# Optimization experiments

Hardware: AMD Instinct MI355X
Metric: run time of the kernel (lower is better)

The kernel has to match this reference:

```python
import jax, jax.numpy as jnp
import numpy as np

B, S, V, F, H = 256, 512, 50000, 64, 256


def setup_inputs() -> dict:
    key = jax.random.key(0)
    ks = jax.random.split(key, 12)
    s_in = 1.0 / np.sqrt(F)
    s_hid = 1.0 / np.sqrt(H)
    return {
        "batch": jax.random.randint(ks[0], (B, S), 0, V),
        "features": jax.random.normal(ks[1], (V, F), jnp.float32),
        "W_ih0": jax.random.normal(ks[2], (H, F), jnp.float32) * s_in,
        "W_hh0": jax.random.normal(ks[3], (H, H), jnp.float32) * s_hid,
        "b_ih0": jax.random.normal(ks[4], (H,), jnp.float32) * s_hid,
        "b_hh0": jax.random.normal(ks[5], (H,), jnp.float32) * s_hid,
        "W_ih1": jax.random.normal(ks[6], (H, H), jnp.float32) * s_hid,
        "W_hh1": jax.random.normal(ks[7], (H, H), jnp.float32) * s_hid,
        "b_ih1": jax.random.normal(ks[8], (H,), jnp.float32) * s_hid,
        "b_hh1": jax.random.normal(ks[9], (H,), jnp.float32) * s_hid,
        "W_out": jax.random.normal(ks[10], (V, H), jnp.float32) * s_hid,
        "b_out": jax.random.normal(ks[11], (V,), jnp.float32) * s_hid,
    }


def _rnn_layer(x, W_ih, W_hh, b_ih, b_hh):
    # x: [B, S, Din] -> [B, S, H]; torch tanh RNN: h_t = tanh(x_t W_ih^T + b_ih + h_{t-1} W_hh^T + b_hh)
    xW = jnp.einsum('bsd,hd->bsh', x, W_ih) + (b_ih + b_hh)  # precompute input projection
    h0 = jnp.zeros((x.shape[0], W_hh.shape[0]), x.dtype)

    def step(h, xt):
        h = jnp.tanh(xt + h @ W_hh.T)
        return h, h

    _, ys = jax.lax.scan(step, h0, jnp.swapaxes(xW, 0, 1))  # scan over time
    return jnp.swapaxes(ys, 0, 1)


def reference(batch, features, W_ih0, W_hh0, b_ih0, b_hh0,
              W_ih1, W_hh1, b_ih1, b_hh1, W_out, b_out):
    # vectorized replacement of the nested per-token gather loop
    full_representation = features[batch]            # [B, S, F]
    h = _rnn_layer(full_representation, W_ih0, W_hh0, b_ih0, b_hh0)
    h = _rnn_layer(h, W_ih1, W_hh1, b_ih1, b_hh1)    # [B, S, H]
    return h[:, -1, :] @ W_out.T + b_out             # [B, V]
```

## Files before the change

### kernel.cpp

```cpp
#include <hip/hip_runtime.h>

#define B_ 256
#define S_ 512
#define V_ 50000
#define F_ 64
#define H_ 256

typedef _Float16 f16;
typedef _Float16 f16x2 __attribute__((ext_vector_type(2)));
typedef _Float16 f16x4 __attribute__((ext_vector_type(4)));
typedef _Float16 f16x8 __attribute__((ext_vector_type(8)));
typedef float f32x4 __attribute__((ext_vector_type(4)));

#define MFMA(a, b, c) __builtin_amdgcn_mfma_f32_16x16x32_f16((a), (b), (c), 0, 0, 0)

__device__ __forceinline__ f16x8 cvt8(const float4 a, const float4 b) {
    f16x8 v;
    v[0] = (f16)a.x; v[1] = (f16)a.y; v[2] = (f16)a.z; v[3] = (f16)a.w;
    v[4] = (f16)b.x; v[5] = (f16)b.y; v[6] = (f16)b.z; v[7] = (f16)b.w;
    return v;
}

__device__ __forceinline__ float fast_tanh(float x) {
    float e = __expf(2.f * x);
    float r = __builtin_amdgcn_rcpf(e + 1.f);
    return __builtin_fmaf(-2.f, r, 1.f);
}

__device__ __forceinline__ f32x4 cvt4f(const f16x4 v) {
    f32x4 r; r[0] = (float)v[0]; r[1] = (float)v[1]; r[2] = (float)v[2]; r[3] = (float)v[3];
    return r;
}
__device__ __forceinline__ f16x4 pack4(const f32x4 a, const f32x4 b) {
    f16x4 r; r[0] = (f16)(a[0] + b[0]); r[1] = (f16)(a[1] + b[1]);
    r[2] = (f16)(a[2] + b[2]); r[3] = (f16)(a[3] + b[3]);
    return r;
}
__device__ __forceinline__ f16x4 tanh4(const f32x4 a, const f32x4 b) {
    f16x4 r;
#pragma unroll
    for (int i = 0; i < 4; ++i) r[i] = (f16)fast_tanh(a[i] + b[i]);
    return r;
}

__global__ void k_init_flags(int* flags) {
    if (threadIdx.x < 128) flags[threadIdx.x] = 0;
}

__global__ __launch_bounds__(512) void k_vocab_proj(
    const float* __restrict__ feat, const float* __restrict__ Wih,
    const float* __restrict__ bi, const float* __restrict__ bh,
    f16* __restrict__ T)
{
    __shared__ char Wl[256 * 128];
    __shared__ char Xl[16 * 128];
    const int tid = threadIdx.x;
    {
        const int n = tid >> 1, k0 = (tid & 1) << 5;
#pragma unroll
        for (int k = k0; k < k0 + 32; k += 8) {
            float4 a = *(const float4*)(Wih + n * F_ + k);
            float4 b = *(const float4*)(Wih + n * F_ + k + 4);
            *(f16x8*)(Wl + n * 128 + (((k >> 3) ^ (n & 7)) << 4)) = cvt8(a, b);
        }
    }
    const int v0 = blockIdx.x * 16;
    {
        const int m = tid >> 5, k = (tid & 31) << 1;
        float2 a = *(const float2*)(feat + (v0 + m) * F_ + k);
        f16x2 v; v[0] = (f16)a.x; v[1] = (f16)a.y;
        *(f16x2*)(Xl + m * 128 + ((((k >> 3) ^ (m & 7)) << 4) | ((k & 7) << 1))) = v;
    }
    __syncthreads();
    const int lane = tid & 63, w = tid >> 6;
    const int q = lane & 15, g = lane >> 4;
#pragma unroll
    for (int nt = 0; nt < 2; ++nt) {
        const int n0 = w * 32 + nt * 16;
        const int nrow = n0 + q;
        float4 b1 = *(const float4*)(bi + n0 + g * 4);
        float4 b2 = *(const float4*)(bh + n0 + g * 4);
        f32x4 acc = {b1.x + b2.x, b1.y + b2.y, b1.z + b2.z, b1.w + b2.w};
#pragma unroll
        for (int kb = 0; kb < 2; ++kb) {
            f16x8 a = *(const f16x8*)(Wl + nrow * 128 + (((kb * 4 + g) ^ (nrow & 7)) << 4));
            f16x8 b = *(const f16x8*)(Xl + q * 128 + (((kb * 4 + g) ^ (q & 7)) << 4));
            acc = MFMA(a, b, acc);
        }
        f16x4 o; o[0] = (f16)acc[0]; o[1] = (f16)acc[1]; o[2] = (f16)acc[2]; o[3] = (f16)acc[3];
        *(f16x4*)(T + (size_t)(v0 + q) * H_ + n0 + g * 4) = o;
    }
}

__global__ __launch_bounds__(512) __attribute__((amdgpu_waves_per_eu(2, 2)))
void k_rnn_split(
    const f16* __restrict__ T, const int* __restrict__ idx,
    const float* __restrict__ Whh0, const float* __restrict__ Wih1,
    const float* __restrict__ bih1, const float* __restrict__ bhh1,
    const float* __restrict__ Whh1,
    f16* __restrict__ pbuf, int* flags, f16* __restrict__ h1out)
{
    __shared__ char hb[2][8192];
    const int wg = blockIdx.x;
    const int tid = threadIdx.x, lane = tid & 63, w = tid >> 6;
    const int q = lane & 15, g = lane >> 4;
    const int ncol = w * 32;
    const int swz = (q & 7) << 4;

    int rbase[2], wbase[2];
#pragma unroll
    for (int p2 = 0; p2 < 2; ++p2)
        rbase[p2] = q * 512 + ((p2 * 64 + g * 16) ^ swz);
#pragma unroll
    for (int tt = 0; tt < 2; ++tt)
        wbase[tt] = q * 512 + (((ncol + tt * 16 + g * 4) * 2) ^ swz);

    const int pr = (wg < 16) ? wg : wg - 16;
    const int brow = pr * 16 + q;
    const size_t prow = (size_t)brow * 512;

#define FRD(kb_, RD_) (*(const f16x8*)(hb[RD_] + rbase[(kb_) & 1] + (((kb_) >> 1) * 128)))
#define HWR(tt_, WR_) (*(f16x4*)(hb[WR_] + wbase[tt_]))
#define STEP_BAR() do { \
        asm volatile("s_waitcnt lgkmcnt(0)" ::: "memory"); \
        __builtin_amdgcn_s_barrier(); \
    } while (0)

    if (wg < 16) {
        f16x8 wA[2][8], wP[2][8];
#pragma unroll
        for (int tt = 0; tt < 2; ++tt) {
            const int n = ncol + tt * 16 + q;
#pragma unroll
            for (int kb = 0; kb < 8; ++kb) {
                const int o = n * H_ + kb * 32 + g * 8;
                wA[tt][kb] = cvt8(*(const float4*)(Whh0 + o), *(const float4*)(Whh0 + o + 4));
                wP[tt][kb] = cvt8(*(const float4*)(Wih1 + o), *(const float4*)(Wih1 + o + 4));
            }
        }
        f32x4 bs1[2];
#pragma unroll
        for (int tt = 0; tt < 2; ++tt) {
            const int n = ncol + tt * 16 + g * 4;
            float4 x = *(const float4*)(bih1 + n);
            float4 y = *(const float4*)(bhh1 + n);
            bs1[tt][0] = x.x + y.x; bs1[tt][1] = x.y + y.y;
            bs1[tt][2] = x.z + y.z; bs1[tt][3] = x.w + y.w;
        }
        {
            f32x4 z = {0.f, 0.f, 0.f, 0.f};
            *(f32x4*)(hb[1] + tid * 16) = z;
        }
        const int* idxr = idx + brow * S_;
        int* myflag = flags + wg * 8 + w;
        f16x4 xa[2], xb[2];
        {
            const size_t r0 = (size_t)idxr[0] * H_, r1 = (size_t)idxr[1] * H_;
#pragma unroll
            for (int tt = 0; tt < 2; ++tt) {
                xa[tt] = *(const f16x4*)(T + r0 + ncol + tt * 16 + g * 4);
                xb[tt] = *(const f16x4*)(T + r1 + ncol + tt * 16 + g * 4);
            }
        }
        int iA = idxr[2], iB = idxr[3];
        __syncthreads();

#define PBODY(XV, ID, RD, WR, T_) do {                                          \
                \
        f16x8 bf0 = FRD(0, RD), bf1 = FRD(1, RD), bf2 = FRD(2, RD),             \
              bf3 = FRD(3, RD), bf4 = FRD(4, RD), bf5 = FRD(5, RD),             \
              bf6 = FRD(6, RD), bf7 = FRD(7, RD);                               \
        f32x4 aL[2], aH[2];                                                     \
        _Pragma("unroll")                                                       \
        for (int tt = 0; tt < 2; ++tt) {                                        \
            aL[tt] = cvt4f(XV[tt]);                                             \
            aH[tt][0] = 0.f; aH[tt][1] = 0.f; aH[tt][2] = 0.f; aH[tt][3] = 0.f; \
        }                                                                       \
        {                 \
            const size_t rr = (size_t)ID * H_;                                  \
            _Pragma("unroll")                                                   \
            for (int tt = 0; tt < 2; ++tt)                                      \
                XV[tt] = *(const f16x4*)(T + rr + ncol + tt * 16 + g * 4);      \
            const int t4 = ((T_) + 4 < S_) ? (T_) + 4 : S_ - 1;                 \
            ID = idxr[t4];                                                      \
        }                                                                       \
                                               \
        _Pragma("unroll")                                                       \
        for (int tt = 0; tt < 2; ++tt) {                                        \
            aL[tt] = MFMA(wA[tt][0], bf0, aL[tt]);                              \
            aH[tt] = MFMA(wA[tt][4], bf4, aH[tt]);                              \
            aL[tt] = MFMA(wA[tt][1], bf1, aL[tt]);                              \
            aH[tt] = MFMA(wA[tt][5], bf5, aH[tt]);                              \
            aL[tt] = MFMA(wA[tt][2], bf2, aL[tt]);                              \
            aH[tt] = MFMA(wA[tt][6], bf6, aH[tt]);                              \
            aL[tt] = MFMA(wA[tt][3], bf3, aL[tt]);                              \
            aH[tt] = MFMA(wA[tt][7], bf7, aH[tt]);                              \
        }                                                                       \
                                  \
        _Pragma("unroll")                                                       \
        for (int tt = 0; tt < 2; ++tt) HWR(tt, WR) = tanh4(aL[tt], aH[tt]);     \
                  \
        f32x4 pL[2], pH[2];                                                     \
        _Pragma("unroll")                                                       \
        for (int tt = 0; tt < 2; ++tt) {                                        \
            pL[tt] = bs1[tt];                                                   \
            pH[tt][0] = 0.f; pH[tt][1] = 0.f; pH[tt][2] = 0.f; pH[tt][3] = 0.f; \
            pL[tt] = MFMA(wP[tt][0], bf0, pL[tt]);                              \
            pH[tt] = MFMA(wP[tt][4], bf4, pH[tt]);                              \
            pL[tt] = MFMA(wP[tt][1], bf1, pL[tt]);                              \
            pH[tt] = MFMA(wP[tt][5], bf5, pH[tt]);                              \
            pL[tt] = MFMA(wP[tt][2], bf2, pL[tt]);                              \
            pH[tt] = MFMA(wP[tt][6], bf6, pH[tt]);                              \
            pL[tt] = MFMA(wP[tt][3], bf3, pL[tt]);                              \
            pH[tt] = MFMA(wP[tt][7], bf7, pH[tt]);                              \
            *(f16x4*)(pbuf + (prow + (T_) - 1) * 256 + ncol + tt * 16 + g * 4)  \
                = pack4(pL[tt], pH[tt]);                                        \
        }                                                                       \
        if ((((T_) & 7) == 0) && lane == 0)                                     \
            __hip_atomic_store(myflag, (T_), __ATOMIC_RELEASE,                  \
                               __HIP_MEMORY_SCOPE_AGENT);                       \
        STEP_BAR();                                                             \
    } while (0)

        {
            f16x8 bf0 = FRD(0, 1), bf1 = FRD(1, 1), bf2 = FRD(2, 1), bf3 = FRD(3, 1),
                  bf4 = FRD(4, 1), bf5 = FRD(5, 1), bf6 = FRD(6, 1), bf7 = FRD(7, 1);
            f32x4 aL[2], aH[2];
#pragma unroll
            for (int tt = 0; tt < 2; ++tt) {
                aL[tt] = cvt4f(xa[tt]);
                aH[tt][0] = 0.f; aH[tt][1] = 0.f; aH[tt][2] = 0.f; aH[tt][3] = 0.f;
            }
            {
                const size_t rr = (size_t)iA * H_;
#pragma unroll
                for (int tt = 0; tt < 2; ++tt)
                    xa[tt] = *(const f16x4*)(T + rr + ncol + tt * 16 + g * 4);
                iA = idxr[4];
            }
#pragma unroll
            for (int tt = 0; tt < 2; ++tt) {
                aL[tt] = MFMA(wA[tt][0], bf0, aL[tt]);
                aH[tt] = MFMA(wA[tt][4], bf4, aH[tt]);
                aL[tt] = MFMA(wA[tt][1], bf1, aL[tt]);
                aH[tt] = MFMA(wA[tt][5], bf5, aH[tt]);
                aL[tt] = MFMA(wA[tt][2], bf2, aL[tt]);
                aH[tt] = MFMA(wA[tt][6], bf6, aH[tt]);
                aL[tt] = MFMA(wA[tt][3], bf3, aL[tt]);
                aH[tt] = MFMA(wA[tt][7], bf7, aH[tt]);
                HWR(tt, 0) = tanh4(aL[tt], aH[tt]);
            }
            STEP_BAR();
        }
        for (int t = 1; t < 511; t += 2) {
            PBODY(xb, iB, 0, 1, t);
            PBODY(xa, iA, 1, 0, t + 1);
        }
        PBODY(xb, iB, 0, 1, 511);
        {
            f16x8 bf0 = FRD(0, 1), bf1 = FRD(1, 1), bf2 = FRD(2, 1), bf3 = FRD(3, 1),
                  bf4 = FRD(4, 1), bf5 = FRD(5, 1), bf6 = FRD(6, 1), bf7 = FRD(7, 1);
            f32x4 pL[2], pH[2];
#pragma unroll
            for (int tt = 0; tt < 2; ++tt) {
                pL[tt] = bs1[tt];
                pH[tt][0] = 0.f; pH[tt][1] = 0.f; pH[tt][2] = 0.f; pH[tt][3] = 0.f;
                pL[tt] = MFMA(wP[tt][0], bf0, pL[tt]);
                pH[tt] = MFMA(wP[tt][4], bf4, pH[tt]);
                pL[tt] = MFMA(wP[tt][1], bf1, pL[tt]);
                pH[tt] = MFMA(wP[tt][5], bf5, pH[tt]);
                pL[tt] = MFMA(wP[tt][2], bf2, pL[tt]);
                pH[tt] = MFMA(wP[tt][6], bf6, pH[tt]);
                pL[tt] = MFMA(wP[tt][3], bf3, pL[tt]);
                pH[tt] = MFMA(wP[tt][7], bf7, pH[tt]);
                *(f16x4*)(pbuf + (prow + 511) * 256 + ncol + tt * 16 + g * 4)
                    = pack4(pL[tt], pH[tt]);
            }
        }
        if (lane == 0)
            __hip_atomic_store(myflag, 512, __ATOMIC_RELEASE, __HIP_MEMORY_SCOPE_AGENT);
#undef PBODY
    } else {
        f16x8 wC[2][8];
#pragma unroll
        for (int tt = 0; tt < 2; ++tt) {
            const int n = ncol + tt * 16 + q;
#pragma unroll
            for (int kb = 0; kb < 8; ++kb) {
                const int o = n * H_ + kb * 32 + g * 8;
                wC[tt][kb] = cvt8(*(const float4*)(Whh1 + o), *(const float4*)(Whh1 + o + 4));
            }
        }
        {   f32x4 z = {0.f, 0.f, 0.f, 0.f}; *(f32x4*)(hb[1] + tid * 16) = z; }
        const int* fl = flags + pr * 8;
        __syncthreads();

#define SPIN(need) do {                                                         \
        int mn;                                                                 \
        do {                                                                    \
            mn = 0x7fffffff;                                                    \
            _Pragma("unroll")                                                   \
            for (int i = 0; i < 8; ++i) {                                       \
                int v = __hip_atomic_load(fl + i, __ATOMIC_RELAXED,             \
                                          __HIP_MEMORY_SCOPE_AGENT);            \
                mn = v < mn ? v : mn;                                           \
            }                                                                   \
        } while (mn < (need));                                                  \
        __builtin_amdgcn_fence(__ATOMIC_ACQUIRE, "agent");                      \
    } while (0)

#define CBODY(PV, RD, WR, T_) do {                                              \
        f16x8 cf0 = FRD(0, RD), cf1 = FRD(1, RD), cf2 = FRD(2, RD),             \
              cf3 = FRD(3, RD), cf4 = FRD(4, RD), cf5 = FRD(5, RD),             \
              cf6 = FRD(6, RD), cf7 = FRD(7, RD);                               \
        f32x4 aL[2], aH[2];                                                     \
        _Pragma("unroll")                                                       \
        for (int tt = 0; tt < 2; ++tt) {                                        \
            aL[tt] = cvt4f(PV[tt]);                                             \
            aH[tt][0] = 0.f; aH[tt][1] = 0.f; aH[tt][2] = 0.f; aH[tt][3] = 0.f; \
        }                                                                       \
        {                                                                       \
            const int tr = ((T_) + 2 < S_) ? (T_) + 2 : S_ - 1;                 \
            _Pragma("unroll")                                                   \
            for (int tt = 0; tt < 2; ++tt)                                      \
                PV[tt] = *(const f16x4*)(pbuf + (prow + tr) * 256 + ncol + tt * 16 + g * 4); \
        }                                                                       \
        _Pragma("unroll")                                                       \
        for (int tt = 0; tt < 2; ++tt) {                                        \
            aL[tt] = MFMA(wC[tt][0], cf0, aL[tt]);                              \
            aH[tt] = MFMA(wC[tt][4], cf4, aH[tt]);                              \
            aL[tt] = MFMA(wC[tt][1], cf1, aL[tt]);                              \
            aH[tt] = MFMA(wC[tt][5], cf5, aH[tt]);                              \
            aL[tt] = MFMA(wC[tt][2], cf2, aL[tt]);                              \
            aH[tt] = MFMA(wC[tt][6], cf6, aH[tt]);                              \
            aL[tt] = MFMA(wC[tt][3], cf3, aL[tt]);                              \
            aH[tt] = MFMA(wC[tt][7], cf7, aH[tt]);                              \
        }                                                                       \
        _Pragma("unroll")                                                       \
        for (int tt = 0; tt < 2; ++tt) {                                        \
            f16x4 hv = tanh4(aL[tt], aH[tt]);                                   \
            HWR(tt, WR) = hv;                                                   \
            if ((T_) == S_ - 1)                                                 \
                *(f16x4*)(h1out + (size_t)brow * H_ + ncol + tt * 16 + g * 4) = hv; \
        }                                                                       \
        STEP_BAR();                                                             \
    } while (0)

        f16x4 pa[2], pb[2];
        SPIN(6);
#pragma unroll
        for (int tt = 0; tt < 2; ++tt) {
            pa[tt] = *(const f16x4*)(pbuf + (prow + 0) * 256 + ncol + tt * 16 + g * 4);
            pb[tt] = *(const f16x4*)(pbuf + (prow + 1) * 256 + ncol + tt * 16 + g * 4);
        }
        for (int tb = 0; tb < 512; tb += 4) {
            if (tb) {
                const int need = (tb + 6 < 512) ? tb + 6 : 512;
                SPIN(need);
            }
            CBODY(pa, 1, 0, tb);
            CBODY(pb, 0, 1, tb + 1);
            CBODY(pa, 1, 0, tb + 2);
            CBODY(pb, 0, 1, tb + 3);
        }
#undef CBODY
#undef SPIN
    }
#undef FRD
#undef HWR
#undef STEP_BAR
}

__global__ __launch_bounds__(512) void k_out(
    const f16* __restrict__ h1, const float* __restrict__ Wout,
    const float* __restrict__ bout, float* __restrict__ out)
{
    __shared__ char Hl[256 * 512];
    const int tid = threadIdx.x;
    {
        const int m = tid >> 1, half = tid & 1;
#pragma unroll
        for (int i = 0; i < 16; ++i) {
            const int blk = half * 16 + i;
            f16x8 v = *(const f16x8*)(h1 + m * H_ + blk * 8);
            *(f16x8*)(Hl + m * 512 + ((blk ^ (m & 7)) << 4)) = v;
        }
    }
    __syncthreads();
    const int lane = tid & 63, w = tid >> 6;
    const int q = lane & 15, g = lane >> 4;
    const int v0 = blockIdx.x * 80;
    f32x4 acc[5][2];
#pragma unroll
    for (int vt = 0; vt < 5; ++vt) {
        float4 bo = *(const float4*)(bout + v0 + vt * 16 + g * 4);
#pragma unroll
        for (int bt = 0; bt < 2; ++bt) {
            acc[vt][bt][0] = bo.x; acc[vt][bt][1] = bo.y;
            acc[vt][bt][2] = bo.z; acc[vt][bt][3] = bo.w;
        }
    }
#pragma unroll
    for (int kb = 0; kb < 8; ++kb) {
        f16x8 bf[2];
#pragma unroll
        for (int bt = 0; bt < 2; ++bt) {
            const int mrow = (w * 2 + bt) * 16 + q;
            bf[bt] = *(const f16x8*)(Hl + mrow * 512 + (((kb * 4 + g) ^ (mrow & 7)) << 4));
        }
#pragma unroll
        for (int vt = 0; vt < 5; ++vt) {
            const size_t vrow = v0 + vt * 16 + q;
            float4 a = *(const float4*)(Wout + vrow * H_ + kb * 32 + g * 8);
            float4 b = *(const float4*)(Wout + vrow * H_ + kb * 32 + g * 8 + 4);
            f16x8 af = cvt8(a, b);
#pragma unroll
            for (int bt = 0; bt < 2; ++bt)
                acc[vt][bt] = MFMA(af, bf[bt], acc[vt][bt]);
        }
    }
#pragma unroll
    for (int vt = 0; vt < 5; ++vt)
#pragma unroll
        for (int bt = 0; bt < 2; ++bt) {
            const int b = (w * 2 + bt) * 16 + q;
            const int v = v0 + vt * 16 + g * 4;
            float4 o = {acc[vt][bt][0], acc[vt][bt][1], acc[vt][bt][2], acc[vt][bt][3]};
            *(float4*)(out + (size_t)b * V_ + v) = o;
        }
}

extern "C" void kernel_launch(void* const* d_in, const int* in_sizes, int n_in,
                              void* d_out, int out_size, void* d_ws, size_t ws_size,
                              hipStream_t stream) {
    (void)in_sizes; (void)n_in; (void)out_size; (void)ws_size;
    const int*   batch = (const int*)  d_in[0];
    const float* feat  = (const float*)d_in[1];
    const float* Wih0  = (const float*)d_in[2];
    const float* Whh0  = (const float*)d_in[3];
    const float* bih0  = (const float*)d_in[4];
    const float* bhh0  = (const float*)d_in[5];
    const float* Wih1  = (const float*)d_in[6];
    const float* Whh1  = (const float*)d_in[7];
    const float* bih1  = (const float*)d_in[8];
    const float* bhh1  = (const float*)d_in[9];
    const float* Wout  = (const float*)d_in[10];
    const float* bout  = (const float*)d_in[11];
    float* out = (float*)d_out;

    f16* T     = (f16*)d_out;
    int* flags = (int*)((char*)d_out + 48000000);
    f16* pbuf  = (f16*)d_ws;
    f16* h1out = (f16*)((char*)d_ws + (size_t)B_ * S_ * H_ * 2);

    k_init_flags<<<dim3(1), dim3(128), 0, stream>>>(flags);
    k_vocab_proj<<<dim3(V_ / 16), dim3(512), 0, stream>>>(feat, Wih0, bih0, bhh0, T);
    k_rnn_split<<<dim3(32), dim3(512), 0, stream>>>(T, batch, Whh0, Wih1, bih1, bhh1,
                                                    Whh1, pbuf, flags, h1out);
    k_out<<<dim3(625), dim3(512), 0, stream>>>(h1out, Wout, bout, out);
}
```

Before: 934.5 us.

## Move layer-1 input projection to consumer blocks via bounded h0 ring buffer

Layer-0 producer blocks now only run the recurrent W_hh0 step and write h0 into a 128-slot ring buffer per batch group, instead of also computing the W_ih1 projection and storing it to a full-sequence buffer. Consumer blocks are split into two halves. Four waves compute the layer-1 input projection from the ring and pass it to the other four through shared memory, and those four run the W_hh1 recurrence. Producer/consumer flags give bidirectional backpressure, which shortens the producer's critical step. In exchange the consumer step gains a second barrier-coupled stage and the ring-slot reuse adds extra synchronization.

```diff
diff --git a/kernel.cpp b/kernel.cpp
--- a/kernel.cpp
+++ b/kernel.cpp
@@ -31,9 +31,8 @@
     f32x4 r; r[0] = (float)v[0]; r[1] = (float)v[1]; r[2] = (float)v[2]; r[3] = (float)v[3];
     return r;
 }
-__device__ __forceinline__ f16x4 pack4(const f32x4 a, const f32x4 b) {
-    f16x4 r; r[0] = (f16)(a[0] + b[0]); r[1] = (f16)(a[1] + b[1]);
-    r[2] = (f16)(a[2] + b[2]); r[3] = (f16)(a[3] + b[3]);
+__device__ __forceinline__ f16x4 pack4s(const f32x4 a) {
+    f16x4 r; r[0] = (f16)a[0]; r[1] = (f16)a[1]; r[2] = (f16)a[2]; r[3] = (f16)a[3];
     return r;
 }
 __device__ __forceinline__ f16x4 tanh4(const f32x4 a, const f32x4 b) {
@@ -44,7 +43,7 @@
 }
 
 __global__ void k_init_flags(int* flags) {
-    if (threadIdx.x < 128) flags[threadIdx.x] = 0;
+    if (threadIdx.x < 256) flags[threadIdx.x] = 0;
 }
 
 __global__ __launch_bounds__(512) void k_vocab_proj(
@@ -93,80 +92,76 @@
 }
 
 __global__ __launch_bounds__(512) __attribute__((amdgpu_waves_per_eu(2, 2)))
-void k_rnn_split(
+void k_rnn2(
     const f16* __restrict__ T, const int* __restrict__ idx,
     const float* __restrict__ Whh0, const float* __restrict__ Wih1,
     const float* __restrict__ bih1, const float* __restrict__ bhh1,
     const float* __restrict__ Whh1,
-    f16* __restrict__ pbuf, int* flags, f16* __restrict__ h1out)
+    f16* __restrict__ h0ring, int* flags, f16* __restrict__ h1out)
 {
     __shared__ char hb[2][8192];
+    __shared__ char pb[2][8192];
     const int wg = blockIdx.x;
     const int tid = threadIdx.x, lane = tid & 63, w = tid >> 6;
-    const int q = lane & 15, g = lane >> 4;
-    const int ncol = w * 32;
+    const int q = lane & 15, gl = lane >> 4;
     const int swz = (q & 7) << 4;
 
-    int rbase[2], wbase[2];
+    int rbase[2];
 #pragma unroll
     for (int p2 = 0; p2 < 2; ++p2)
-        rbase[p2] = q * 512 + ((p2 * 64 + g * 16) ^ swz);
-#pragma unroll
-    for (int tt = 0; tt < 2; ++tt)
-        wbase[tt] = q * 512 + (((ncol + tt * 16 + g * 4) * 2) ^ swz);
-
-    const int pr = (wg < 16) ? wg : wg - 16;
-    const int brow = pr * 16 + q;
-    const size_t prow = (size_t)brow * 512;
+        rbase[p2] = q * 512 + ((p2 * 64 + gl * 16) ^ swz);
+
+    int* prodf = flags;
+    int* consf = flags + 128;
+    const int gr = (wg < 16) ? wg : wg - 16;
+    const int brow = gr * 16 + q;
+    f16* ringg = h0ring + ((size_t)gr << 19);
 
 #define FRD(kb_, RD_) (*(const f16x8*)(hb[RD_] + rbase[(kb_) & 1] + (((kb_) >> 1) * 128)))
-#define HWR(tt_, WR_) (*(f16x4*)(hb[WR_] + wbase[tt_]))
 #define STEP_BAR() do { \
         asm volatile("s_waitcnt lgkmcnt(0)" ::: "memory"); \
         __builtin_amdgcn_s_barrier(); \
     } while (0)
 
     if (wg < 16) {
-        f16x8 wA[2][8], wP[2][8];
+        const int nb2 = w * 32;
+        int wb2[2];
+#pragma unroll
+        for (int tt = 0; tt < 2; ++tt)
+            wb2[tt] = q * 512 + (((nb2 + tt * 16 + gl * 4) * 2) ^ swz);
+
+        f16x8 wA[2][8];
 #pragma unroll
         for (int tt = 0; tt < 2; ++tt) {
-            const int n = ncol + tt * 16 + q;
+            const int n = nb2 + tt * 16 + q;
 #pragma unroll
             for (int kb = 0; kb < 8; ++kb) {
-                const int o = n * H_ + kb * 32 + g * 8;
+                const int o = n * H_ + kb * 32 + gl * 8;
                 wA[tt][kb] = cvt8(*(const float4*)(Whh0 + o), *(const float4*)(Whh0 + o + 4));
-                wP[tt][kb] = cvt8(*(const float4*)(Wih1 + o), *(const float4*)(Wih1 + o + 4));
-            }
-        }
-        f32x4 bs1[2];
-#pragma unroll
-        for (int tt = 0; tt < 2; ++tt) {
-            const int n = ncol + tt * 16 + g * 4;
-            float4 x = *(const float4*)(bih1 + n);
-            float4 y = *(const float4*)(bhh1 + n);
-            bs1[tt][0] = x.x + y.x; bs1[tt][1] = x.y + y.y;
-            bs1[tt][2] = x.z + y.z; bs1[tt][3] = x.w + y.w;
-        }
-        {
-            f32x4 z = {0.f, 0.f, 0.f, 0.f};
-            *(f32x4*)(hb[1] + tid * 16) = z;
-        }
+            }
+        }
+        {   f32x4 z = {0.f, 0.f, 0.f, 0.f}; *(f32x4*)(hb[1] + tid * 16) = z; }
         const int* idxr = idx + brow * S_;
-        int* myflag = flags + wg * 8 + w;
+        int* myflag = prodf + gr * 8 + w;
         f16x4 xa[2], xb[2];
         {
             const size_t r0 = (size_t)idxr[0] * H_, r1 = (size_t)idxr[1] * H_;
 #pragma unroll
             for (int tt = 0; tt < 2; ++tt) {
-                xa[tt] = *(const f16x4*)(T + r0 + ncol + tt * 16 + g * 4);
-                xb[tt] = *(const f16x4*)(T + r1 + ncol + tt * 16 + g * 4);
+                xa[tt] = *(const f16x4*)(T + r0 + nb2 + tt * 16 + gl * 4);
+                xb[tt] = *(const f16x4*)(T + r1 + nb2 + tt * 16 + gl * 4);
             }
         }
         int iA = idxr[2], iB = idxr[3];
         __syncthreads();
 
 #define PBODY(XV, ID, RD, WR, T_) do {                                          \
-                \
+        if (((T_) & 15) == 0) {       \
+            int v_;                                                             \
+            do { v_ = __hip_atomic_load(consf + gr, __ATOMIC_RELAXED,           \
+                                        __HIP_MEMORY_SCOPE_AGENT);              \
+            } while ((T_) - v_ > 96);                                           \
+        }                                                                       \
         f16x8 bf0 = FRD(0, RD), bf1 = FRD(1, RD), bf2 = FRD(2, RD),             \
               bf3 = FRD(3, RD), bf4 = FRD(4, RD), bf5 = FRD(5, RD),             \
               bf6 = FRD(6, RD), bf7 = FRD(7, RD);                               \
@@ -176,15 +171,18 @@
             aL[tt] = cvt4f(XV[tt]);                                             \
             aH[tt][0] = 0.f; aH[tt][1] = 0.f; aH[tt][2] = 0.f; aH[tt][3] = 0.f; \
         }                                                                       \
-        {                 \
+                    \
+        if ((((T_) & 7) == 0) && lane == 0)                                     \
+            __hip_atomic_store(myflag, (T_), __ATOMIC_RELEASE,                  \
+                               __HIP_MEMORY_SCOPE_AGENT);                       \
+        {                                                                       \
             const size_t rr = (size_t)ID * H_;                                  \
             _Pragma("unroll")                                                   \
             for (int tt = 0; tt < 2; ++tt)                                      \
-                XV[tt] = *(const f16x4*)(T + rr + ncol + tt * 16 + g * 4);      \
+                XV[tt] = *(const f16x4*)(T + rr + nb2 + tt * 16 + gl * 4);      \
             const int t4 = ((T_) + 4 < S_) ? (T_) + 4 : S_ - 1;                 \
             ID = idxr[t4];                                                      \
         }                                                                       \
-                                               \
         _Pragma("unroll")                                                       \
         for (int tt = 0; tt < 2; ++tt) {                                        \
             aL[tt] = MFMA(wA[tt][0], bf0, aL[tt]);                              \
@@ -196,29 +194,15 @@
             aL[tt] = MFMA(wA[tt][3], bf3, aL[tt]);                              \
             aH[tt] = MFMA(wA[tt][7], bf7, aH[tt]);                              \
         }                                                                       \
-                                  \
-        _Pragma("unroll")                                                       \
-        for (int tt = 0; tt < 2; ++tt) HWR(tt, WR) = tanh4(aL[tt], aH[tt]);     \
-                  \
-        f32x4 pL[2], pH[2];                                                     \
-        _Pragma("unroll")                                                       \
-        for (int tt = 0; tt < 2; ++tt) {                                        \
-            pL[tt] = bs1[tt];                                                   \
-            pH[tt][0] = 0.f; pH[tt][1] = 0.f; pH[tt][2] = 0.f; pH[tt][3] = 0.f; \
-            pL[tt] = MFMA(wP[tt][0], bf0, pL[tt]);                              \
-            pH[tt] = MFMA(wP[tt][4], bf4, pH[tt]);                              \
-            pL[tt] = MFMA(wP[tt][1], bf1, pL[tt]);                              \
-            pH[tt] = MFMA(wP[tt][5], bf5, pH[tt]);                              \
-            pL[tt] = MFMA(wP[tt][2], bf2, pL[tt]);                              \
-            pH[tt] = MFMA(wP[tt][6], bf6, pH[tt]);                              \
-            pL[tt] = MFMA(wP[tt][3], bf3, pL[tt]);                              \
-            pH[tt] = MFMA(wP[tt][7], bf7, pH[tt]);                              \
-            *(f16x4*)(pbuf + (prow + (T_) - 1) * 256 + ncol + tt * 16 + g * 4)  \
-                = pack4(pL[tt], pH[tt]);                                        \
+        {                                                                       \
+            f16* rp = ringg + (size_t)((T_) & 127) * 4096 + q * 256 + nb2;      \
+            _Pragma("unroll")                                                   \
+            for (int tt = 0; tt < 2; ++tt) {                                    \
+                f16x4 hv = tanh4(aL[tt], aH[tt]);                               \
+                *(f16x4*)(hb[WR] + wb2[tt]) = hv;                               \
+                *(f16x4*)(rp + tt * 16 + gl * 4) = hv;                          \
+            }                                                                   \
         }                                                                       \
-        if ((((T_) & 7) == 0) && lane == 0)                                     \
-            __hip_atomic_store(myflag, (T_), __ATOMIC_RELEASE,                  \
-                               __HIP_MEMORY_SCOPE_AGENT);                       \
         STEP_BAR();                                                             \
     } while (0)
 
@@ -235,7 +219,7 @@
                 const size_t rr = (size_t)iA * H_;
 #pragma unroll
                 for (int tt = 0; tt < 2; ++tt)
-                    xa[tt] = *(const f16x4*)(T + rr + ncol + tt * 16 + g * 4);
+                    xa[tt] = *(const f16x4*)(T + rr + nb2 + tt * 16 + gl * 4);
                 iA = idxr[4];
             }
 #pragma unroll
@@ -248,7 +232,13 @@
                 aH[tt] = MFMA(wA[tt][6], bf6, aH[tt]);
                 aL[tt] = MFMA(wA[tt][3], bf3, aL[tt]);
                 aH[tt] = MFMA(wA[tt][7], bf7, aH[tt]);
-                HWR(tt, 0) = tanh4(aL[tt], aH[tt]);
+            }
+            f16* rp = ringg + q * 256 + nb2;
+#pragma unroll
+            for (int tt = 0; tt < 2; ++tt) {
+                f16x4 hv = tanh4(aL[tt], aH[tt]);
+                *(f16x4*)(hb[0] + wb2[tt]) = hv;
+                *(f16x4*)(rp + tt * 16 + gl * 4) = hv;
             }
             STEP_BAR();
         }
@@ -257,117 +247,183 @@
             PBODY(xa, iA, 1, 0, t + 1);
         }
         PBODY(xb, iB, 0, 1, 511);
-        {
-            f16x8 bf0 = FRD(0, 1), bf1 = FRD(1, 1), bf2 = FRD(2, 1), bf3 = FRD(3, 1),
-                  bf4 = FRD(4, 1), bf5 = FRD(5, 1), bf6 = FRD(6, 1), bf7 = FRD(7, 1);
-            f32x4 pL[2], pH[2];
-#pragma unroll
-            for (int tt = 0; tt < 2; ++tt) {
-                pL[tt] = bs1[tt];
-                pH[tt][0] = 0.f; pH[tt][1] = 0.f; pH[tt][2] = 0.f; pH[tt][3] = 0.f;
-                pL[tt] = MFMA(wP[tt][0], bf0, pL[tt]);
-                pH[tt] = MFMA(wP[tt][4], bf4, pH[tt]);
-                pL[tt] = MFMA(wP[tt][1], bf1, pL[tt]);
-                pH[tt] = MFMA(wP[tt][5], bf5, pH[tt]);
-                pL[tt] = MFMA(wP[tt][2], bf2, pL[tt]);
-                pH[tt] = MFMA(wP[tt][6], bf6, pH[tt]);
-                pL[tt] = MFMA(wP[tt][3], bf3, pL[tt]);
-                pH[tt] = MFMA(wP[tt][7], bf7, pH[tt]);
-                *(f16x4*)(pbuf + (prow + 511) * 256 + ncol + tt * 16 + g * 4)
-                    = pack4(pL[tt], pH[tt]);
-            }
-        }
         if (lane == 0)
-            __hip_atomic_store(myflag, 512, __ATOMIC_RELEASE, __HIP_MEMORY_SCOPE_AGENT);
+            __hip_atomic_store(myflag, 516, __ATOMIC_RELEASE, __HIP_MEMORY_SCOPE_AGENT);
 #undef PBODY
     } else {
-        f16x8 wC[2][8];
-#pragma unroll
-        for (int tt = 0; tt < 2; ++tt) {
-            const int n = ncol + tt * 16 + q;
-#pragma unroll
-            for (int kb = 0; kb < 8; ++kb) {
-                const int o = n * H_ + kb * 32 + g * 8;
-                wC[tt][kb] = cvt8(*(const float4*)(Whh1 + o), *(const float4*)(Whh1 + o + 4));
-            }
-        }
-        {   f32x4 z = {0.f, 0.f, 0.f, 0.f}; *(f32x4*)(hb[1] + tid * 16) = z; }
-        const int* fl = flags + pr * 8;
-        __syncthreads();
+        const bool isC = (w < 4);
+        const int nb4 = (isC ? w : w - 4) * 64;
+        int xbase[4];
+#pragma unroll
+        for (int tt = 0; tt < 4; ++tt)
+            xbase[tt] = q * 512 + (((nb4 + tt * 16 + gl * 4) * 2) ^ swz);
+
+        f16x8 wR[4][8];
+        {
+            const float* Wsrc = isC ? Whh1 : Wih1;
+#pragma unroll
+            for (int tt = 0; tt < 4; ++tt) {
+                const int n = nb4 + tt * 16 + q;
+#pragma unroll
+                for (int kb = 0; kb < 8; ++kb) {
+                    const int o = n * H_ + kb * 32 + gl * 8;
+                    wR[tt][kb] = cvt8(*(const float4*)(Wsrc + o), *(const float4*)(Wsrc + o + 4));
+                }
+            }
+        }
+        f32x4 bs1[4];
+#pragma unroll
+        for (int tt = 0; tt < 4; ++tt) {
+            const int n = nb4 + tt * 16 + gl * 4;
+            float4 x = *(const float4*)(bih1 + n);
+            float4 y = *(const float4*)(bhh1 + n);
+            bs1[tt][0] = x.x + y.x; bs1[tt][1] = x.y + y.y;
+            bs1[tt][2] = x.z + y.z; bs1[tt][3] = x.w + y.w;
+        }
+        {
+            f32x4 z = {0.f, 0.f, 0.f, 0.f};
+            *(f32x4*)(hb[1] + tid * 16) = z;
+        }
 
 #define SPIN(need) do {                                                         \
-        int mn;                                                                 \
+        int mn_;                                                                \
         do {                                                                    \
-            mn = 0x7fffffff;                                                    \
-            _Pragma("unroll")                                                   \
-            for (int i = 0; i < 8; ++i) {                                       \
-                int v = __hip_atomic_load(fl + i, __ATOMIC_RELAXED,             \
-                                          __HIP_MEMORY_SCOPE_AGENT);            \
-                mn = v < mn ? v : mn;                                           \
-            }                                                                   \
-        } while (mn < (need));                                                  \
+            mn_ = 0x7fffffff;                                                   \
+            _Pragma("unroll")                                                   \
+            for (int i_ = 0; i_ < 8; ++i_) {                                    \
+                int v_ = __hip_atomic_load(prodf + gr * 8 + i_, __ATOMIC_RELAXED, \
+                                           __HIP_MEMORY_SCOPE_AGENT);           \
+                mn_ = v_ < mn_ ? v_ : mn_;                                      \
+            }                                                                   \
+        } while (mn_ < (need));                                                 \
         __builtin_amdgcn_fence(__ATOMIC_ACQUIRE, "agent");                      \
     } while (0)
 
-#define CBODY(PV, RD, WR, T_) do {                                              \
-        f16x8 cf0 = FRD(0, RD), cf1 = FRD(1, RD), cf2 = FRD(2, RD),             \
-              cf3 = FRD(3, RD), cf4 = FRD(4, RD), cf5 = FRD(5, RD),             \
-              cf6 = FRD(6, RD), cf7 = FRD(7, RD);                               \
-        f32x4 aL[2], aH[2];                                                     \
-        _Pragma("unroll")                                                       \
-        for (int tt = 0; tt < 2; ++tt) {                                        \
-            aL[tt] = cvt4f(PV[tt]);                                             \
-            aH[tt][0] = 0.f; aH[tt][1] = 0.f; aH[tt][2] = 0.f; aH[tt][3] = 0.f; \
-        }                                                                       \
-        {                                                                       \
-            const int tr = ((T_) + 2 < S_) ? (T_) + 2 : S_ - 1;                 \
-            _Pragma("unroll")                                                   \
-            for (int tt = 0; tt < 2; ++tt)                                      \
-                PV[tt] = *(const f16x4*)(pbuf + (prow + tr) * 256 + ncol + tt * 16 + g * 4); \
-        }                                                                       \
-        _Pragma("unroll")                                                       \
-        for (int tt = 0; tt < 2; ++tt) {                                        \
-            aL[tt] = MFMA(wC[tt][0], cf0, aL[tt]);                              \
-            aH[tt] = MFMA(wC[tt][4], cf4, aH[tt]);                              \
-            aL[tt] = MFMA(wC[tt][1], cf1, aL[tt]);                              \
-            aH[tt] = MFMA(wC[tt][5], cf5, aH[tt]);                              \
-            aL[tt] = MFMA(wC[tt][2], cf2, aL[tt]);                              \
-            aH[tt] = MFMA(wC[tt][6], cf6, aH[tt]);                              \
-            aL[tt] = MFMA(wC[tt][3], cf3, aL[tt]);                              \
-            aH[tt] = MFMA(wC[tt][7], cf7, aH[tt]);                              \
-        }                                                                       \
-        _Pragma("unroll")                                                       \
-        for (int tt = 0; tt < 2; ++tt) {                                        \
-            f16x4 hv = tanh4(aL[tt], aH[tt]);                                   \
-            HWR(tt, WR) = hv;                                                   \
-            if ((T_) == S_ - 1)                                                 \
-                *(f16x4*)(h1out + (size_t)brow * H_ + ncol + tt * 16 + g * 4) = hv; \
+        f16x8 HF[8];
+        if (!isC) {
+            SPIN(12);
+            const f16* rp = ringg + q * 256 + gl * 8;
+#pragma unroll
+            for (int kb = 0; kb < 8; ++kb)
+                HF[kb] = *(const f16x8*)(rp + kb * 32);
+        }
+        __syncthreads();
+
+#define SBODY(WRP, RDP, WRH, RDH, S_) do {                                      \
+        if (isC) {                                                              \
+            f16x8 cf0 = FRD(0, RDH), cf1 = FRD(1, RDH), cf2 = FRD(2, RDH),      \
+                  cf3 = FRD(3, RDH), cf4 = FRD(4, RDH), cf5 = FRD(5, RDH),      \
+                  cf6 = FRD(6, RDH), cf7 = FRD(7, RDH);                         \
+            f32x4 cL[4], cH[4];                                                 \
+            _Pragma("unroll")                                                   \
+            for (int tt = 0; tt < 4; ++tt) {                                    \
+                f16x4 pv = *(const f16x4*)(pb[RDP] + xbase[tt]);                \
+                cL[tt] = cvt4f(pv);                                             \
+                cH[tt][0] = 0.f; cH[tt][1] = 0.f; cH[tt][2] = 0.f; cH[tt][3] = 0.f; \
+            }                                                                   \
+            _Pragma("unroll")                                                   \
+            for (int tt = 0; tt < 4; ++tt) {                                    \
+                cL[tt] = MFMA(wR[tt][0], cf0, cL[tt]);                          \
+                cH[tt] = MFMA(wR[tt][4], cf4, cH[tt]);                          \
+                cL[tt] = MFMA(wR[tt][1], cf1, cL[tt]);                          \
+                cH[tt] = MFMA(wR[tt][5], cf5, cH[tt]);                          \
+                cL[tt] = MFMA(wR[tt][2], cf2, cL[tt]);                          \
+                cH[tt] = MFMA(wR[tt][6], cf6, cH[tt]);                          \
+                cL[tt] = MFMA(wR[tt][3], cf3, cL[tt]);                          \
+                cH[tt] = MFMA(wR[tt][7], cf7, cH[tt]);                          \
+            }                                                                   \
+            _Pragma("unroll")                                                   \
+            for (int tt = 0; tt < 4; ++tt)                                      \
+                *(f16x4*)(hb[WRH] + xbase[tt]) = tanh4(cL[tt], cH[tt]);         \
+            if ((tid == 0) && (((S_) & 15) == 0))                               \
+                __hip_atomic_store(consf + gr, (S_), __ATOMIC_RELEASE,          \
+                                   __HIP_MEMORY_SCOPE_AGENT);                   \
+        } else {                                                                \
+            if (((S_) & 7) == 0) {                                              \
+                const int nd_ = ((S_) + 12 < 512) ? (S_) + 12 : 512;            \
+                SPIN(nd_);                                                      \
+            }                                                                   \
+            f32x4 pA[4];                                                        \
+            _Pragma("unroll")                                                   \
+            for (int tt = 0; tt < 4; ++tt) pA[tt] = bs1[tt];                    \
+            _Pragma("unroll")                                                   \
+            for (int kb = 0; kb < 8; ++kb) {                                    \
+                _Pragma("unroll")                                               \
+                for (int tt = 0; tt < 4; ++tt)                                  \
+                    pA[tt] = MFMA(wR[tt][kb], HF[kb], pA[tt]);                  \
+            }                                                                   \
+            {   \
+                const int nx = ((S_) + 1 < 512) ? (S_) + 1 : 511;               \
+                const f16* rp = ringg + (size_t)(nx & 127) * 4096 + q * 256 + gl * 8; \
+                _Pragma("unroll")                                               \
+                for (int kb = 0; kb < 8; ++kb)                                  \
+                    HF[kb] = *(const f16x8*)(rp + kb * 32);                     \
+            }                                                                   \
+            _Pragma("unroll")                                                   \
+            for (int tt = 0; tt < 4; ++tt)                                      \
+                *(f16x4*)(pb[WRP] + xbase[tt]) = pack4s(pA[tt]);                \
         }                                                                       \
         STEP_BAR();                                                             \
     } while (0)
 
-        f16x4 pa[2], pb[2];
-        SPIN(6);
-#pragma unroll
-        for (int tt = 0; tt < 2; ++tt) {
-            pa[tt] = *(const f16x4*)(pbuf + (prow + 0) * 256 + ncol + tt * 16 + g * 4);
-            pb[tt] = *(const f16x4*)(pbuf + (prow + 1) * 256 + ncol + tt * 16 + g * 4);
-        }
-        for (int tb = 0; tb < 512; tb += 4) {
-            if (tb) {
-                const int need = (tb + 6 < 512) ? tb + 6 : 512;
-                SPIN(need);
-            }
-            CBODY(pa, 1, 0, tb);
-            CBODY(pb, 0, 1, tb + 1);
-            CBODY(pa, 1, 0, tb + 2);
-            CBODY(pb, 0, 1, tb + 3);
-        }
-#undef CBODY
+        {
+            if (!isC) {
+                f32x4 pA[4];
+#pragma unroll
+                for (int tt = 0; tt < 4; ++tt) pA[tt] = bs1[tt];
+#pragma unroll
+                for (int kb = 0; kb < 8; ++kb) {
+#pragma unroll
+                    for (int tt = 0; tt < 4; ++tt)
+                        pA[tt] = MFMA(wR[tt][kb], HF[kb], pA[tt]);
+                }
+                {
+                    const f16* rp = ringg + 4096 + q * 256 + gl * 8;
+#pragma unroll
+                    for (int kb = 0; kb < 8; ++kb)
+                        HF[kb] = *(const f16x8*)(rp + kb * 32);
+                }
+#pragma unroll
+                for (int tt = 0; tt < 4; ++tt)
+                    *(f16x4*)(pb[0] + xbase[tt]) = pack4s(pA[tt]);
+            }
+            STEP_BAR();
+        }
+        for (int s = 1; s < 511; s += 2) {
+            SBODY(1, 0, 0, 1, s);
+            SBODY(0, 1, 1, 0, s + 1);
+        }
+        SBODY(1, 0, 0, 1, 511);
+        if (isC) {
+            f16x8 cf0 = FRD(0, 0), cf1 = FRD(1, 0), cf2 = FRD(2, 0), cf3 = FRD(3, 0),
+                  cf4 = FRD(4, 0), cf5 = FRD(5, 0), cf6 = FRD(6, 0), cf7 = FRD(7, 0);
+            f32x4 cL[4], cH[4];
+#pragma unroll
+            for (int tt = 0; tt < 4; ++tt) {
+                f16x4 pv = *(const f16x4*)(pb[1] + xbase[tt]);
+                cL[tt] = cvt4f(pv);
+                cH[tt][0] = 0.f; cH[tt][1] = 0.f; cH[tt][2] = 0.f; cH[tt][3] = 0.f;
+            }
+#pragma unroll
+            for (int tt = 0; tt < 4; ++tt) {
+                cL[tt] = MFMA(wR[tt][0], cf0, cL[tt]);
+                cH[tt] = MFMA(wR[tt][4], cf4, cH[tt]);
+                cL[tt] = MFMA(wR[tt][1], cf1, cL[tt]);
+                cH[tt] = MFMA(wR[tt][5], cf5, cH[tt]);
+                cL[tt] = MFMA(wR[tt][2], cf2, cL[tt]);
+                cH[tt] = MFMA(wR[tt][6], cf6, cH[tt]);
+                cL[tt] = MFMA(wR[tt][3], cf3, cL[tt]);
+                cH[tt] = MFMA(wR[tt][7], cf7, cH[tt]);
+            }
+#pragma unroll
+            for (int tt = 0; tt < 4; ++tt)
+                *(f16x4*)(h1out + (size_t)brow * H_ + nb4 + tt * 16 + gl * 4)
+                    = tanh4(cL[tt], cH[tt]);
+        }
+#undef SBODY
 #undef SPIN
     }
 #undef FRD
-#undef HWR
 #undef STEP_BAR
 }
 
@@ -448,14 +504,14 @@
     const float* bout  = (const float*)d_in[11];
     float* out = (float*)d_out;
 
-    f16* T     = (f16*)d_out;
-    int* flags = (int*)((char*)d_out + 48000000);
-    f16* pbuf  = (f16*)d_ws;
-    f16* h1out = (f16*)((char*)d_ws + (size_t)B_ * S_ * H_ * 2);
-
-    k_init_flags<<<dim3(1), dim3(128), 0, stream>>>(flags);
+    f16* T      = (f16*)d_out;
+    f16* h0ring = (f16*)((char*)d_out + 27000000);
+    int* flags  = (int*)((char*)d_out + 48000000);
+    f16* h1out  = (f16*)d_ws;
+
+    k_init_flags<<<dim3(1), dim3(256), 0, stream>>>(flags);
     k_vocab_proj<<<dim3(V_ / 16), dim3(512), 0, stream>>>(feat, Wih0, bih0, bhh0, T);
-    k_rnn_split<<<dim3(32), dim3(512), 0, stream>>>(T, batch, Whh0, Wih1, bih1, bhh1,
-                                                    Whh1, pbuf, flags, h1out);
+    k_rnn2<<<dim3(32), dim3(512), 0, stream>>>(T, batch, Whh0, Wih1, bih1, bhh1,
+                                               Whh1, h0ring, flags, h1out);
     k_out<<<dim3(625), dim3(512), 0, stream>>>(h1out, Wout, bout, out);
 }
```

Result: faster. 864.3 us (median of 3 runs) (-7.5%).
